# Performance work log

Hardware: AMD Instinct MI355X
Metric: run time of the kernel (lower is better)

## Reference

```python
import jax, jax.numpy as jnp
import numpy as np

NUM_CLASSES = 27
LAM_U, LAM_B, LAM_D = 0.3, 0.2, 0.2


def _grads(x2d):
    # backward-difference with edge replication (matches torch.cat([x[:, :, :1], x[:, :, :-1]]))
    gx = x2d - jnp.concatenate([x2d[:, :, :1], x2d[:, :, :-1]], axis=-1)
    gy = x2d - jnp.concatenate([x2d[:, :1, :], x2d[:, :-1, :]], axis=-2)
    return gx, gy


def setup_inputs() -> dict:
    key = jax.random.key(0)
    k1, k2, k3 = jax.random.split(key, 3)
    B, M, H, W = 16, 32, 256, 256
    N = H * W
    return {
        "semantic_pred": jax.random.randint(k1, (B, N), 0, NUM_CLASSES, dtype=jnp.int32),
        "instance_masks": jax.random.uniform(k2, (B, M, N), dtype=jnp.float32),
        "depth": jax.random.uniform(k3, (B, N), dtype=jnp.float32),
        "spatial_h": H,
        "spatial_w": W,
    }


def _forward(semantic_pred, instance_masks, depth, spatial_h, spatial_w):
    b, m, n = instance_masks.shape

    # ---- uniformity loss: fused one-hot matmul replaces B*M*C python loops ----
    onehot = jax.nn.one_hot(semantic_pred, NUM_CLASSES, dtype=instance_masks.dtype)  # (B,N,C)
    class_hist = jnp.einsum('bmn,bnc->bmc', instance_masks, onehot)                  # (B,M,C)
    mask_sum = jnp.sum(instance_masks, axis=-1) + 1e-6                               # (B,M)
    class_prob = jnp.clip(class_hist / mask_sum[..., None], 1e-7, 1.0)
    entropy = -jnp.sum(jnp.where(class_prob > 1e-6,
                                 class_prob * jnp.log(class_prob + 1e-10),
                                 jnp.zeros_like(class_prob)), axis=-1)               # (B,M)
    l_uniform = jnp.sum(entropy) / (b * m + 1e-8)

    # ---- boundary alignment loss ----
    sem_2d = semantic_pred.reshape(b, spatial_h, spatial_w).astype(jnp.float32)
    mask_2d = instance_masks[:, 0, :].reshape(b, spatial_h, spatial_w)
    sgx, sgy = _grads(sem_2d)
    sem_boundary = ((jnp.abs(sgx) > 0) | (jnp.abs(sgy) > 0)).astype(jnp.float32)
    mgx, mgy = _grads(mask_2d)
    inst_boundary = ((jnp.abs(mgx) > 0.3) | (jnp.abs(mgy) > 0.3)).astype(jnp.float32)
    intersection = jnp.sum(sem_boundary * inst_boundary, axis=(-2, -1))
    union = jnp.sum(jnp.maximum(sem_boundary, inst_boundary), axis=(-2, -1)) + 1e-8
    l_boundary = 1.0 - jnp.mean(intersection / union)

    # ---- depth-boundary coherence loss ----
    depth_2d = depth.reshape(b, spatial_h, spatial_w)
    dgx, dgy = _grads(depth_2d)
    s = dgx ** 2 + dgy ** 2
    depth_boundary = jnp.sqrt(jnp.maximum(s, 1e-24))  # eps avoids NaN grad at s==0; forward ~identical
    sem_b = jnp.maximum((sgx != 0).astype(jnp.float32), (sgy != 0).astype(jnp.float32))
    db_clamped = jnp.clip(depth_boundary, 0.0, 2.0)
    weight = 1.0 + db_clamped * 3.0
    l_dbc = jnp.mean(weight * (1.0 - sem_b) * db_clamped)

    total = LAM_U * l_uniform + LAM_B * l_boundary + LAM_D * l_dbc
    return l_uniform, l_boundary, l_dbc, total


def reference(semantic_pred, instance_masks, depth, spatial_h, spatial_w):
    return _forward(semantic_pred, instance_masks, depth, spatial_h, spatial_w)
```

## Files before the change

kernel.cpp:

```cpp
#include <hip/hip_runtime.h>
#include <math.h>

#define NUM_CLASSES 27
#define HDIM 256
#define WDIM 256
#define NPIX (HDIM * WDIM)

#define NB_HIST 512
#define NB_BND 1024
#define ROWS_PER_BND_BLOCK 4


__global__ __launch_bounds__(256) void fused_kernel(
    const float* __restrict__ masks, const int* __restrict__ sem,
    const float* __restrict__ depth, float* __restrict__ ws, int M) {
  __shared__ float s_hist[28][256];
  __shared__ float s_part[8][32];
  __shared__ float s_i[4], s_u[4], s_t[4];

  const int tid = threadIdx.x;

  if (blockIdx.x < NB_HIST) {
    const int bm = blockIdx.x;
    const int b = bm / M;
    const int m = bm % M;

    float* col = &s_hist[0][tid];
#pragma unroll
    for (int c = 0; c < 28; ++c) col[c * 256] = 0.0f;

    const float4* __restrict__ m4 =
        (const float4*)(masks + ((size_t)b * M + m) * (size_t)NPIX);
    const int4* __restrict__ s4 = (const int4*)(sem + (size_t)b * (size_t)NPIX);

    const int iters = NPIX / 4 / 256;
#pragma unroll 4
    for (int it = 0; it < iters; ++it) {
      const int idx = it * 256 + tid;
      const float4 mv = m4[idx];
      const int4 cv = s4[idx];
      col[cv.x * 256] += mv.x;
      col[cv.y * 256] += mv.y;
      col[cv.z * 256] += mv.z;
      col[cv.w * 256] += mv.w;
    }
    __syncthreads();

    {
      const int c = tid & 31;
      const int s = tid >> 5;
      if (c < 28) {
        float acc = 0.f;
#pragma unroll
        for (int i = 0; i < 32; ++i)
          acc += s_hist[c][s * 32 + ((i + c) & 31)];
        s_part[s][c] = acc;
      }
    }
    __syncthreads();

    if (tid < 64) {
      float tot = 0.f;
      if (tid < 28) {
#pragma unroll
        for (int g = 0; g < 8; ++g) tot += s_part[g][tid];
      }
      float ms = tot;
      for (int off = 32; off > 0; off >>= 1) ms += __shfl_xor(ms, off);
      ms += 1e-6f;
      float ent = 0.f;
      if (tid < NUM_CLASSES) {
        float p = fminf(fmaxf(tot / ms, 1e-7f), 1.0f);
        if (p > 1e-6f) ent = p * logf(p + 1e-10f);
      }
      for (int off = 32; off > 0; off >>= 1) ent += __shfl_xor(ent, off);
      if (tid == 0) ws[bm] = -ent;
    }
  } else {
    const int j = blockIdx.x - NB_HIST;
    const int wave = tid >> 6;
    const int lane = tid & 63;
    const int brow = j * ROWS_PER_BND_BLOCK + wave;
    const int b = brow >> 8;
    const int y = brow & 255;

    const size_t rowoff = (size_t)b * NPIX + (size_t)y * WDIM;
    const float4* mp = (const float4*)(masks + (size_t)b * M * NPIX + (size_t)y * WDIM);
    const float4* dp = (const float4*)(depth + rowoff);
    const int4* sp = (const int4*)(sem + rowoff);

    const int uoff = (y > 0) ? -(WDIM / 4) : 0;

    const float4 mv = mp[lane];
    const float4 mvu = mp[lane + uoff];
    const float4 dv = dp[lane];
    const float4 dvu = dp[lane + uoff];
    const int4 sv = sp[lane];
    const int4 svu = sp[lane + uoff];

    const int src = (lane > 0) ? (lane - 1) : 0;
    float mw = __shfl(mv.w, src);
    float dw = __shfl(dv.w, src);
    int swv = __shfl(sv.w, src);
    if (lane == 0) { mw = mv.x; dw = dv.x; swv = sv.x; }

    const float ml[4] = {mw, mv.x, mv.y, mv.z};
    const float dl[4] = {dw, dv.x, dv.y, dv.z};
    const int sl[4] = {swv, sv.x, sv.y, sv.z};
    const float mc[4] = {mv.x, mv.y, mv.z, mv.w};
    const float dc[4] = {dv.x, dv.y, dv.z, dv.w};
    const int sc[4] = {sv.x, sv.y, sv.z, sv.w};
    const float mu[4] = {mvu.x, mvu.y, mvu.z, mvu.w};
    const float du[4] = {dvu.x, dvu.y, dvu.z, dvu.w};
    const int su[4] = {svu.x, svu.y, svu.z, svu.w};

    float inter = 0.f, uni = 0.f, term = 0.f;
#pragma unroll
    for (int k = 0; k < 4; ++k) {
      const bool semb = (sc[k] != sl[k]) || (sc[k] != su[k]);
      const bool instb = (fabsf(mc[k] - ml[k]) > 0.3f) || (fabsf(mc[k] - mu[k]) > 0.3f);
      inter += (semb && instb) ? 1.0f : 0.0f;
      uni += (semb || instb) ? 1.0f : 0.0f;
      const float gx = dc[k] - dl[k];
      const float gy = dc[k] - du[k];
      const float db = sqrtf(fmaxf(gx * gx + gy * gy, 1e-24f));
      const float dbc = fminf(db, 2.0f);
      term += semb ? 0.0f : (1.0f + 3.0f * dbc) * dbc;
    }

    for (int off = 32; off > 0; off >>= 1) {
      inter += __shfl_down(inter, off);
      uni += __shfl_down(uni, off);
      term += __shfl_down(term, off);
    }
    if (lane == 0) { s_i[wave] = inter; s_u[wave] = uni; s_t[wave] = term; }
    __syncthreads();
    if (tid == 0) {
      float bi = 0.f, bu = 0.f, bt = 0.f;
#pragma unroll
      for (int w = 0; w < 4; ++w) { bi += s_i[w]; bu += s_u[w]; bt += s_t[w]; }
      ws[512 + j] = bi;
      ws[1536 + j] = bu;
      ws[2560 + j] = bt;
    }
  }
}

__global__ __launch_bounds__(512) void finalize_kernel(
    const float* __restrict__ ws, float* __restrict__ out, int B, int M) {
  const int tid = threadIdx.x;
  const int lane = tid & 63;
  const int wave = tid >> 6;
  __shared__ float s_e[8], s_d[8], s_r[16];

  float e = ws[tid];
  float inter = ws[512 + 2 * tid] + ws[512 + 2 * tid + 1];
  float uni = ws[1536 + 2 * tid] + ws[1536 + 2 * tid + 1];
  float dbc = ws[2560 + 2 * tid] + ws[2560 + 2 * tid + 1];

  for (int off = 16; off > 0; off >>= 1) {
    inter += __shfl_down(inter, off, 32);
    uni += __shfl_down(uni, off, 32);
  }
  if ((tid & 31) == 0) s_r[tid >> 5] = inter / (uni + 1e-8f);

  for (int off = 32; off > 0; off >>= 1) {
    e += __shfl_down(e, off);
    dbc += __shfl_down(dbc, off);
  }
  if (lane == 0) { s_e[wave] = e; s_d[wave] = dbc; }
  __syncthreads();

  if (tid == 0) {
    float se = 0.f, sd = 0.f, sr = 0.f;
#pragma unroll
    for (int w = 0; w < 8; ++w) { se += s_e[w]; sd += s_d[w]; }
#pragma unroll
    for (int b = 0; b < 16; ++b) sr += s_r[b];
    const float l_u = se / ((float)(B * M) + 1e-8f);
    const float l_b = 1.0f - sr / (float)B;
    const float l_d = sd / (float)((size_t)B * NPIX);
    out[0] = l_u;
    out[1] = l_b;
    out[2] = l_d;
    out[3] = 0.3f * l_u + 0.2f * l_b + 0.2f * l_d;
  }
}

extern "C" void kernel_launch(void* const* d_in, const int* in_sizes, int n_in,
                              void* d_out, int out_size, void* d_ws, size_t ws_size,
                              hipStream_t stream) {
  const int* sem = (const int*)d_in[0];
  const float* masks = (const float*)d_in[1];
  const float* depth = (const float*)d_in[2];

  const int B = in_sizes[0] / NPIX;
  const int M = in_sizes[1] / in_sizes[0];
  float* ws = (float*)d_ws;
  float* out = (float*)d_out;

  fused_kernel<<<NB_HIST + NB_BND, 256, 0, stream>>>(masks, sem, depth, ws, M);
  finalize_kernel<<<1, 512, 0, stream>>>(ws, out, B, M);
}
```

Before: 202.4 us.

## Split histogram blocks into pixel chunks and defer entropy to finalize

Each (batch, instance) histogram is now split across up to four blocks, each covering a chunk of the pixels, which raises the number of histogram blocks from 512 to 2048. Each block writes 28 partial class bins to the workspace, and the finalize kernel sums the chunks and computes the entropy per instance. The goal is better occupancy and load balance on a GPU with many CUs, at the cost of more workspace traffic, a heavier single-block finalize, and dropping the explicit unroll on the accumulation loop.

```diff
diff --git a/kernel.cpp b/kernel.cpp
--- a/kernel.cpp
+++ b/kernel.cpp
@@ -6,43 +6,43 @@
 #define WDIM 256
 #define NPIX (HDIM * WDIM)
 
-#define NB_HIST 512
 #define NB_BND 1024
 #define ROWS_PER_BND_BLOCK 4
 
 
 __global__ __launch_bounds__(256) void fused_kernel(
     const float* __restrict__ masks, const int* __restrict__ sem,
-    const float* __restrict__ depth, float* __restrict__ ws, int M) {
+    const float* __restrict__ depth, float* __restrict__ ws, int M, int nch) {
   __shared__ float s_hist[28][256];
   __shared__ float s_part[8][32];
   __shared__ float s_i[4], s_u[4], s_t[4];
 
   const int tid = threadIdx.x;
-
-  if (blockIdx.x < NB_HIST) {
-    const int bm = blockIdx.x;
+  const int nhb = nch << 9;
+
+  if ((int)blockIdx.x < nhb) {
+    const int bm = blockIdx.x & 511;
+    const int q = blockIdx.x >> 9;
     const int b = bm / M;
     const int m = bm % M;
 
-    float* col = &s_hist[0][tid];
-#pragma unroll
-    for (int c = 0; c < 28; ++c) col[c * 256] = 0.0f;
+#pragma unroll
+    for (int c = 0; c < 28; ++c) s_hist[c][tid] = 0.0f;
 
     const float4* __restrict__ m4 =
         (const float4*)(masks + ((size_t)b * M + m) * (size_t)NPIX);
     const int4* __restrict__ s4 = (const int4*)(sem + (size_t)b * (size_t)NPIX);
 
-    const int iters = NPIX / 4 / 256;
-#pragma unroll 4
-    for (int it = 0; it < iters; ++it) {
+    const int itpc = 64 / nch;
+    const int it0 = q * itpc;
+    for (int it = it0; it < it0 + itpc; ++it) {
       const int idx = it * 256 + tid;
       const float4 mv = m4[idx];
       const int4 cv = s4[idx];
-      col[cv.x * 256] += mv.x;
-      col[cv.y * 256] += mv.y;
-      col[cv.z * 256] += mv.z;
-      col[cv.w * 256] += mv.w;
+      s_hist[cv.x][tid] += mv.x;
+      s_hist[cv.y][tid] += mv.y;
+      s_hist[cv.z][tid] += mv.z;
+      s_hist[cv.w][tid] += mv.w;
     }
     __syncthreads();
 
@@ -59,25 +59,14 @@
     }
     __syncthreads();
 
-    if (tid < 64) {
+    if (tid < 28) {
       float tot = 0.f;
-      if (tid < 28) {
-#pragma unroll
-        for (int g = 0; g < 8; ++g) tot += s_part[g][tid];
-      }
-      float ms = tot;
-      for (int off = 32; off > 0; off >>= 1) ms += __shfl_xor(ms, off);
-      ms += 1e-6f;
-      float ent = 0.f;
-      if (tid < NUM_CLASSES) {
-        float p = fminf(fmaxf(tot / ms, 1e-7f), 1.0f);
-        if (p > 1e-6f) ent = p * logf(p + 1e-10f);
-      }
-      for (int off = 32; off > 0; off >>= 1) ent += __shfl_xor(ent, off);
-      if (tid == 0) ws[bm] = -ent;
+#pragma unroll
+      for (int g = 0; g < 8; ++g) tot += s_part[g][tid];
+      ws[((size_t)bm * nch + q) * 28 + tid] = tot;
     }
   } else {
-    const int j = blockIdx.x - NB_HIST;
+    const int j = blockIdx.x - nhb;
     const int wave = tid >> 6;
     const int lane = tid & 63;
     const int brow = j * ROWS_PER_BND_BLOCK + wave;
@@ -139,24 +128,45 @@
       float bi = 0.f, bu = 0.f, bt = 0.f;
 #pragma unroll
       for (int w = 0; w < 4; ++w) { bi += s_i[w]; bu += s_u[w]; bt += s_t[w]; }
-      ws[512 + j] = bi;
-      ws[1536 + j] = bu;
-      ws[2560 + j] = bt;
+      const int nbase = nhb * 28;
+      ws[nbase + j] = bi;
+      ws[nbase + 1024 + j] = bu;
+      ws[nbase + 2048 + j] = bt;
     }
   }
 }
 
 __global__ __launch_bounds__(512) void finalize_kernel(
-    const float* __restrict__ ws, float* __restrict__ out, int B, int M) {
+    const float* __restrict__ ws, float* __restrict__ out, int B, int M, int nch) {
   const int tid = threadIdx.x;
   const int lane = tid & 63;
   const int wave = tid >> 6;
   __shared__ float s_e[8], s_d[8], s_r[16];
 
-  float e = ws[tid];
-  float inter = ws[512 + 2 * tid] + ws[512 + 2 * tid + 1];
-  float uni = ws[1536 + 2 * tid] + ws[1536 + 2 * tid + 1];
-  float dbc = ws[2560 + 2 * tid] + ws[2560 + 2 * tid + 1];
+  float bins[28];
+#pragma unroll
+  for (int c = 0; c < 28; ++c) bins[c] = 0.f;
+  for (int q = 0; q < nch; ++q) {
+    const size_t base = ((size_t)tid * nch + q) * 28;
+#pragma unroll
+    for (int c = 0; c < 28; ++c) bins[c] += ws[base + c];
+  }
+  float ms = 0.f;
+#pragma unroll
+  for (int c = 0; c < 28; ++c) ms += bins[c];
+  ms += 1e-6f;
+  float ent = 0.f;
+#pragma unroll
+  for (int c = 0; c < NUM_CLASSES; ++c) {
+    const float p = fminf(fmaxf(bins[c] / ms, 1e-7f), 1.0f);
+    if (p > 1e-6f) ent += p * logf(p + 1e-10f);
+  }
+  float e = -ent;
+
+  const int nbase = (nch << 9) * 28;
+  float inter = ws[nbase + 2 * tid] + ws[nbase + 2 * tid + 1];
+  float uni = ws[nbase + 1024 + 2 * tid] + ws[nbase + 1024 + 2 * tid + 1];
+  float dbc = ws[nbase + 2048 + 2 * tid] + ws[nbase + 2048 + 2 * tid + 1];
 
   for (int off = 16; off > 0; off >>= 1) {
     inter += __shfl_down(inter, off, 32);
@@ -199,6 +209,8 @@
   float* ws = (float*)d_ws;
   float* out = (float*)d_out;
 
-  fused_kernel<<<NB_HIST + NB_BND, 256, 0, stream>>>(masks, sem, depth, ws, M);
-  finalize_kernel<<<1, 512, 0, stream>>>(ws, out, B, M);
+  const int nch = (ws_size >= 60416u * sizeof(float)) ? 4 : 1;
+
+  fused_kernel<<<512 * nch + NB_BND, 256, 0, stream>>>(masks, sem, depth, ws, M, nch);
+  finalize_kernel<<<1, 512, 0, stream>>>(ws, out, B, M, nch);
 }
```

Measured after the change: 214.2 us. 5.9% more time.
